# Optimization experiments

Measured on AMD Instinct MI355X. Metric: run time of the kernel, lower is better.

The kernel has to match this reference:

```python
import jax, jax.numpy as jnp
import numpy as np

B, NNODE, E = 262144, 5, 8
NF, EF, D, ED = 7, 2, 16, 4
L = 4  # num_convs
INV = 1.0 / np.sqrt(1.0 + 1e-5)  # BN eval with running_mean=0, running_var=1


def setup_inputs() -> dict:
    key = jax.random.key(0)
    ks = iter(jax.random.split(key, 64))
    r = lambda shape, s=0.1: s * jax.random.normal(next(ks), shape, dtype=jnp.float32)
    g = lambda shape: 1.0 + 0.1 * jax.random.normal(next(ks), shape, dtype=jnp.float32)
    inp = {}
    inp['node_feat'] = jax.random.normal(next(ks), (B, NNODE, NF), dtype=jnp.float32)
    inp['edge_feat'] = jax.random.normal(next(ks), (B, E, EF), dtype=jnp.float32)
    inp['edge_index'] = jax.random.randint(next(ks), (2, E), 0, NNODE)
    # embeddings
    inp['W_ne'] = r((NF, D)); inp['b_ne'] = r((D,))
    inp['g_ne'] = g((NNODE,)); inp['be_ne'] = r((NNODE,))
    inp['W_ee'] = r((EF, ED)); inp['b_ee'] = r((ED,))
    # conv layers (stacked over L)
    inp['msg_W1'] = r((L, 2 * D + ED, D)); inp['msg_b1'] = r((L, D))
    inp['msg_W2'] = r((L, D, D)); inp['msg_b2'] = r((L, D))
    inp['upd_W1'] = r((L, 2 * D, D)); inp['upd_b1'] = r((L, D))
    inp['upd_g1'] = g((L, NNODE)); inp['upd_be1'] = r((L, NNODE))
    inp['upd_W2'] = r((L, D, D)); inp['upd_b2'] = r((L, D))
    inp['upd_g2'] = g((L, NNODE)); inp['upd_be2'] = r((L, NNODE))
    # pool
    inp['Wp'] = r((NNODE * D, D)); inp['bp'] = r((D,))
    inp['gp'] = g((D,)); inp['bep'] = r((D,))
    # MLP head
    inp['mlp_W1'] = r((D, 64)); inp['mlp_b1'] = r((64,)); inp['mlp_g1'] = g((64,)); inp['mlp_be1'] = r((64,))
    inp['mlp_W2'] = r((64, 64)); inp['mlp_b2'] = r((64,)); inp['mlp_g2'] = g((64,)); inp['mlp_be2'] = r((64,))
    inp['mlp_W3'] = r((64, 64)); inp['mlp_b3'] = r((64,)); inp['mlp_g3'] = g((64,)); inp['mlp_be3'] = r((64,))
    inp['mlp_W4'] = r((64, 1)); inp['mlp_b4'] = r((1,))
    return inp


def _bn5(x, gam, bet):  # x: [B,5,D], BatchNorm1d(5) eval over channel dim 1
    return gam[None, :, None] * (x * INV) + bet[None, :, None]


def _bnc(x, gam, bet):  # x: [N,C]
    return gam * (x * INV) + bet


def reference(node_feat, edge_feat, edge_index, W_ne, b_ne, g_ne, be_ne, W_ee, b_ee,
              msg_W1, msg_b1, msg_W2, msg_b2, upd_W1, upd_b1, upd_g1, upd_be1,
              upd_W2, upd_b2, upd_g2, upd_be2, Wp, bp, gp, bep,
              mlp_W1, mlp_b1, mlp_g1, mlp_be1, mlp_W2, mlp_b2, mlp_g2, mlp_be2,
              mlp_W3, mlp_b3, mlp_g3, mlp_be3, mlp_W4, mlp_b4):
    src, dst = edge_index[0], edge_index[1]
    x = _bn5(node_feat @ W_ne + b_ne, g_ne, be_ne)          # [B,5,D]
    ea = edge_feat @ W_ee + b_ee                             # [B,E,ED]
    cnt = jnp.zeros((NNODE,), jnp.float32).at[dst].add(1.0)
    denom = jnp.clip(cnt, 1.0)[None, :, None]
    for l in range(L):
        h_i = x[:, dst, :]                                   # [B,E,D] dest gather
        h_j = x[:, src, :]                                   # [B,E,D] source gather
        m = jnp.concatenate([h_i, h_j, ea], axis=-1)         # [B,E,2D+ED]
        m = jax.nn.sigmoid(m @ msg_W1[l] + msg_b1[l])
        m = jax.nn.sigmoid(m @ msg_W2[l] + msg_b2[l])        # [B,E,D]
        agg = jnp.zeros_like(x).at[:, dst, :].add(m) / denom  # mean scatter -> [B,5,D]
        u = jnp.concatenate([x, agg], axis=-1)               # [B,5,2D]
        u = jax.nn.sigmoid(_bn5(u @ upd_W1[l] + upd_b1[l], upd_g1[l], upd_be1[l]))
        u = jax.nn.sigmoid(_bn5(u @ upd_W2[l] + upd_b2[l], upd_g2[l], upd_be2[l]))
        x = x + u                                            # residual
    p = x.reshape(x.shape[0], NNODE * D)                     # concat of 5 node slots
    p = jax.nn.sigmoid(_bnc(p @ Wp + bp, gp, bep))
    p = jax.nn.sigmoid(_bnc(p @ mlp_W1 + mlp_b1, mlp_g1, mlp_be1))
    p = jax.nn.sigmoid(_bnc(p @ mlp_W2 + mlp_b2, mlp_g2, mlp_be2))
    p = jax.nn.sigmoid(_bnc(p @ mlp_W3 + mlp_b3, mlp_g3, mlp_be3))
    return p @ mlp_W4 + mlp_b4                               # [B,1]
```

## Files before the change

### kernel.cpp

```cpp
#include <hip/hip_runtime.h>

#define NT 256
#define GPB 64
#define NB 262144
#define NCOL 66
#define ROWS 128
#define INVC 0.9999950000374997f

typedef __attribute__((ext_vector_type(8))) short bf8;
typedef __attribute__((ext_vector_type(4))) float f4;

struct P {
  const float* node_feat; const float* edge_feat; const int* ei;
  const float* W_ne; const float* b_ne; const float* g_ne; const float* be_ne;
  const float* W_ee; const float* b_ee;
  const float* msg_W1; const float* msg_b1; const float* msg_W2; const float* msg_b2;
  const float* upd_W1; const float* upd_b1; const float* upd_g1; const float* upd_be1;
  const float* upd_W2; const float* upd_b2; const float* upd_g2; const float* upd_be2;
  const float* Wp; const float* bp; const float* gp; const float* bep;
  const float* mW1; const float* mb1; const float* mg1; const float* mbe1;
  const float* mW2; const float* mb2; const float* mg2; const float* mbe2;
  const float* mW3; const float* mb3; const float* mg3; const float* mbe3;
  const float* mW4; const float* mb4;
  float* out;
};

__device__ __forceinline__ float sigm(float x) {
  return __builtin_amdgcn_rcpf(1.0f + __expf(-x));
}

__device__ __forceinline__ float bff(short s) {
  return __builtin_bit_cast(float, ((unsigned)(unsigned short)s) << 16);
}

struct F2 { bf8 h, l; };

__device__ __forceinline__ F2 pack2(const float (&v)[8]) {
  F2 r;
#pragma unroll
  for (int i = 0; i < 8; i++) {
    short hi = (short)(__builtin_bit_cast(unsigned, v[i]) >> 16);
    r.h[i] = hi;
    float res = v[i] - bff(hi);
    r.l[i] = (short)(__builtin_bit_cast(unsigned, res) >> 16);
  }
  return r;
}

__device__ __forceinline__ f4 mm(const F2& a, const F2& b, f4 c) {
  c = __builtin_amdgcn_mfma_f32_16x16x32_bf16(a.l, b.h, c, 0, 0, 0);
  c = __builtin_amdgcn_mfma_f32_16x16x32_bf16(a.h, b.l, c, 0, 0, 0);
  c = __builtin_amdgcn_mfma_f32_16x16x32_bf16(a.h, b.h, c, 0, 0, 0);
  return c;
}

template <int KV>
__device__ __forceinline__ F2 packB(const float* W, int LD, int q, int n) {
  float v[8];
#pragma unroll
  for (int i = 0; i < 8; i++) {
    const int kq = 8 * q + i;
    v[i] = (kq < KV) ? W[kq * LD + n] : 0.f;
  }
  return pack2(v);
}

__device__ __forceinline__ F2 packAr(const float* xb, int row0) {
  float v[8];
#pragma unroll
  for (int i = 0; i < 8; i++) v[i] = xb[(row0 + i) * NCOL];
  return pack2(v);
}
__device__ __forceinline__ F2 packA16(const float* xb, int rowbase, int q) {
  float v[8];
#pragma unroll
  for (int i = 0; i < 8; i++) {
    const int k = 8 * q + i;
    v[i] = (k < 16) ? xb[(rowbase + k) * NCOL] : 0.f;
  }
  return pack2(v);
}

__device__ __forceinline__ void wrD(float* dst, f4 d) {
  *(float2*)dst = float2{d[0], d[1]};
  *(float2*)(dst + 2) = float2{d[2], d[3]};
}

__device__ __forceinline__ f4 splat4(float b) { return f4{b, b, b, b}; }

__global__ __launch_bounds__(NT, 1) void gnn_kernel(P pp) {
  __shared__ float xs[ROWS][NCOL];

  const int t = threadIdx.x;
  const int w = t >> 6;
  const int l = t & 63;
  const int q = l >> 4;
  const int m16 = l & 15;
  const int col = w * 16 + m16;
  const int cD = w * 16 + 4 * q;
  const int gbase = blockIdx.x * GPB + w * 16;

  const float* xb = &xs[0][col];
  const f4 z4 = {0.f, 0.f, 0.f, 0.f};

  int se_[8], de_[8];
#pragma unroll
  for (int e = 0; e < 8; e++) {
    se_[e] = __builtin_amdgcn_readfirstlane(pp.ei[e]);
    de_[e] = __builtin_amdgcn_readfirstlane(pp.ei[8 + e]);
  }
  float dr_[5];
#pragma unroll
  for (int n = 0; n < 5; n++) {
    int c = 0;
#pragma unroll
    for (int e = 0; e < 8; e++) c += (de_[e] == n) ? 1 : 0;
    dr_[n] = 1.0f / (float)(c > 1 ? c : 1);
  }

  {
    F2 Bne = packB<7>(pp.W_ne, 16, q, m16);
#pragma unroll 1
    for (int n = 0; n < 5; n++) {
      float v[8];
#pragma unroll
      for (int i = 0; i < 8; i++) {
        const int k = 8 * q + i;
        v[i] = (k < 7) ? pp.node_feat[(size_t)(gbase + m16) * 35 + n * 7 + k] : 0.f;
      }
      F2 a = pack2(v);
      f4 d = mm(a, Bne, z4);
      const float gn = pp.g_ne[n] * INVC, bn = pp.be_ne[n];
      f4 o;
#pragma unroll
      for (int r = 0; r < 4; r++) o[r] = fmaf(gn, d[r], bn);
      wrD(&xs[n * 16 + m16][cD], o);
    }
  }

#pragma unroll 1
  for (int l4 = 0; l4 < 4; l4++) {
    const float* mW1 = pp.msg_W1 + l4 * 576;
    F2 B1a = packB<32>(mW1, 16, q, m16);
    F2 B1e = packB<4>(mW1 + 512, 16, q, m16);
    F2 B2  = packB<16>(pp.msg_W2 + l4 * 256, 16, q, m16);
    F2 BU1 = packB<32>(pp.upd_W1 + l4 * 512, 16, q, m16);
    F2 BU2 = packB<16>(pp.upd_W2 + l4 * 256, 16, q, m16);
    const float mb1n = pp.msg_b1[l4 * 16 + m16];
    const float mb2n = pp.msg_b2[l4 * 16 + m16];
    const float ub1n = pp.upd_b1[l4 * 16 + m16];
    const float ub2n = pp.upd_b2[l4 * 16 + m16];

    f4 agg[5];
#pragma unroll
    for (int n = 0; n < 5; n++) agg[n] = z4;

#pragma unroll 1
    for (int e = 0; e < 8; e++) {
      const int se = se_[e], de = de_[e];

      float v[8] = {0.f, 0.f, 0.f, 0.f, 0.f, 0.f, 0.f, 0.f};
      if (q == 0) {
        const float* ef = pp.edge_feat + (size_t)(gbase + m16) * 16 + 2 * e;
        const float e0 = ef[0], e1 = ef[1];
#pragma unroll
        for (int j = 0; j < 4; j++)
          v[j] = fmaf(e0, pp.W_ee[j], fmaf(e1, pp.W_ee[4 + j], pp.b_ee[j]));
      }
      F2 aea = pack2(v);

      f4 c1 = splat4(mb1n);
      c1 = mm(aea, B1e, c1);
      const int rowH = (q < 2) ? de * 16 + 8 * q : se * 16 + 8 * (q - 2);
      F2 ah = packAr(xb, rowH);
      c1 = mm(ah, B1a, c1);
#pragma unroll
      for (int r = 0; r < 4; r++) c1[r] = sigm(c1[r]);
      wrD(&xs[80 + m16][cD], c1);
      F2 am = packA16(xb, 80, q);

      f4 c2 = splat4(mb2n);
      c2 = mm(am, B2, c2);
#pragma unroll
      for (int r = 0; r < 4; r++) {
        const float vv = sigm(c2[r]);
        agg[0][r] += (de == 0) ? vv : 0.f;
        agg[1][r] += (de == 1) ? vv : 0.f;
        agg[2][r] += (de == 2) ? vv : 0.f;
        agg[3][r] += (de == 3) ? vv : 0.f;
        agg[4][r] += (de == 4) ? vv : 0.f;
      }
    }

#pragma unroll
    for (int nn = 0; nn < 5; nn++) {
      const float dr = dr_[nn];
      f4 av;
#pragma unroll
      for (int r = 0; r < 4; r++) av[r] = agg[nn][r] * dr;
      wrD(&xs[80 + m16][cD], av);
      const int rowU = (q < 2) ? nn * 16 + 8 * q : 80 + 8 * (q - 2);
      F2 au = packAr(xb, rowU);
      f4 c = splat4(ub1n);
      c = mm(au, BU1, c);
      const float G1 = pp.upd_g1[l4 * 5 + nn] * INVC;
      const float Bb1 = pp.upd_be1[l4 * 5 + nn];
#pragma unroll
      for (int r = 0; r < 4; r++) c[r] = sigm(fmaf(G1, c[r], Bb1));
      wrD(&xs[80 + m16][cD], c);
      F2 a2 = packA16(xb, 80, q);
      f4 c2 = splat4(ub2n);
      c2 = mm(a2, BU2, c2);
      const float G2 = pp.upd_g2[l4 * 5 + nn] * INVC;
      const float Bb2 = pp.upd_be2[l4 * 5 + nn];
      float* xp = &xs[nn * 16 + m16][cD];
      float2 x01 = *(float2*)xp;
      float2 x23 = *(float2*)(xp + 2);
      x01.x += sigm(fmaf(G2, c2[0], Bb2));
      x01.y += sigm(fmaf(G2, c2[1], Bb2));
      x23.x += sigm(fmaf(G2, c2[2], Bb2));
      x23.y += sigm(fmaf(G2, c2[3], Bb2));
      *(float2*)xp = x01;
      *(float2*)(xp + 2) = x23;
    }
  }

  {
    f4 c = splat4(pp.bp[m16]);
    F2 a0 = packAr(xb, 8 * q);
    F2 b0 = packB<32>(pp.Wp, 16, q, m16);
    c = mm(a0, b0, c);
    F2 a1 = packAr(xb, 32 + 8 * q);
    F2 b1 = packB<32>(pp.Wp + 512, 16, q, m16);
    c = mm(a1, b1, c);
    F2 a2 = packA16(xb, 64, q);
    F2 b2 = packB<16>(pp.Wp + 1024, 16, q, m16);
    c = mm(a2, b2, c);
    const float gpn = pp.gp[m16] * INVC, bepn = pp.bep[m16];
    f4 o;
#pragma unroll
    for (int r = 0; r < 4; r++) o[r] = sigm(fmaf(gpn, c[r], bepn));
    wrD(&xs[80 + m16][cD], o);
  }

  {
    F2 a = packA16(xb, 80, q);
#pragma unroll 1
    for (int nt = 0; nt < 4; nt++) {
      const int nb = nt * 16 + m16;
      F2 b = packB<16>(pp.mW1 + nt * 16, 64, q, m16);
      f4 c = splat4(pp.mb1[nb]);
      c = mm(a, b, c);
      const float g = pp.mg1[nb] * INVC, be = pp.mbe1[nb];
      f4 o;
#pragma unroll
      for (int r = 0; r < 4; r++) o[r] = sigm(fmaf(g, c[r], be));
      wrD(&xs[nt * 16 + m16][cD], o);
    }
  }
  {
    F2 a0 = packAr(xb, 8 * q);
    F2 a1 = packAr(xb, 32 + 8 * q);
#pragma unroll 1
    for (int nt = 0; nt < 4; nt++) {
      const int nb = nt * 16 + m16;
      F2 b0 = packB<32>(pp.mW2 + nt * 16, 64, q, m16);
      F2 b1 = packB<32>(pp.mW2 + 32 * 64 + nt * 16, 64, q, m16);
      f4 c = splat4(pp.mb2[nb]);
      c = mm(a0, b0, c);
      c = mm(a1, b1, c);
      const float g = pp.mg2[nb] * INVC, be = pp.mbe2[nb];
      f4 o;
#pragma unroll
      for (int r = 0; r < 4; r++) o[r] = sigm(fmaf(g, c[r], be));
      wrD(&xs[64 + nt * 16 + m16][cD], o);
    }
  }
  {
    F2 a0 = packAr(xb, 64 + 8 * q);
    F2 a1 = packAr(xb, 96 + 8 * q);
#pragma unroll 1
    for (int nt = 0; nt < 4; nt++) {
      const int nb = nt * 16 + m16;
      F2 b0 = packB<32>(pp.mW3 + nt * 16, 64, q, m16);
      F2 b1 = packB<32>(pp.mW3 + 32 * 64 + nt * 16, 64, q, m16);
      f4 c = splat4(pp.mb3[nb]);
      c = mm(a0, b0, c);
      c = mm(a1, b1, c);
      const float g = pp.mg3[nb] * INVC, be = pp.mbe3[nb];
      f4 o;
#pragma unroll
      for (int r = 0; r < 4; r++) o[r] = sigm(fmaf(g, c[r], be));
      wrD(&xs[nt * 16 + m16][cD], o);
    }
  }
  {
    float s = 0.f;
#pragma unroll
    for (int j = 0; j < 16; j++)
      s = fmaf(xs[q * 16 + j][col], pp.mW4[q * 16 + j], s);
    s += __shfl_down(s, 32);
    s += __shfl_down(s, 16);
    if (l < 16) pp.out[gbase + m16] = s + pp.mb4[0];
  }
}

extern "C" void kernel_launch(void* const* d_in, const int* in_sizes, int n_in,
                              void* d_out, int out_size, void* d_ws, size_t ws_size,
                              hipStream_t stream) {
  P p;
  p.node_feat = (const float*)d_in[0];
  p.edge_feat = (const float*)d_in[1];
  p.ei        = (const int*)d_in[2];
  p.W_ne  = (const float*)d_in[3];  p.b_ne  = (const float*)d_in[4];
  p.g_ne  = (const float*)d_in[5];  p.be_ne = (const float*)d_in[6];
  p.W_ee  = (const float*)d_in[7];  p.b_ee  = (const float*)d_in[8];
  p.msg_W1 = (const float*)d_in[9];  p.msg_b1 = (const float*)d_in[10];
  p.msg_W2 = (const float*)d_in[11]; p.msg_b2 = (const float*)d_in[12];
  p.upd_W1 = (const float*)d_in[13]; p.upd_b1 = (const float*)d_in[14];
  p.upd_g1 = (const float*)d_in[15]; p.upd_be1 = (const float*)d_in[16];
  p.upd_W2 = (const float*)d_in[17]; p.upd_b2 = (const float*)d_in[18];
  p.upd_g2 = (const float*)d_in[19]; p.upd_be2 = (const float*)d_in[20];
  p.Wp  = (const float*)d_in[21]; p.bp  = (const float*)d_in[22];
  p.gp  = (const float*)d_in[23]; p.bep = (const float*)d_in[24];
  p.mW1 = (const float*)d_in[25]; p.mb1 = (const float*)d_in[26];
  p.mg1 = (const float*)d_in[27]; p.mbe1 = (const float*)d_in[28];
  p.mW2 = (const float*)d_in[29]; p.mb2 = (const float*)d_in[30];
  p.mg2 = (const float*)d_in[31]; p.mbe2 = (const float*)d_in[32];
  p.mW3 = (const float*)d_in[33]; p.mb3 = (const float*)d_in[34];
  p.mg3 = (const float*)d_in[35]; p.mbe3 = (const float*)d_in[36];
  p.mW4 = (const float*)d_in[37]; p.mb4 = (const float*)d_in[38];
  p.out = (float*)d_out;

  hipLaunchKernelGGL(gnn_kernel, dim3(NB / GPB), dim3(NT), 0, stream, p);
}
```

Measured before the change: 337.6 us.

## Store activations in shared memory as pre-split bf16 hi/lo pairs

Shared-memory activations are now stored as packed 32-bit words holding the bf16 high part and the bf16 residual, split once at write time. Building an MFMA fragment then needs only byte permutes instead of a full float-to-bf16x2 split per element on every read. packA16 also skips the loads for the zero-padded quads. The residual state x is kept in this packed form, so each update adds precision loss (effectively about 16 mantissa bits). The row stride also changes from 66 to 64, which may alter LDS bank-conflict behaviour.

Measured after the change: 385.6 us. +14.2%, slower.

```diff
diff --git a/kernel.cpp b/kernel.cpp
--- a/kernel.cpp
+++ b/kernel.cpp
@@ -3,12 +3,14 @@
 #define NT 256
 #define GPB 64
 #define NB 262144
-#define NCOL 66
+#define NCOL 64
 #define ROWS 128
 #define INVC 0.9999950000374997f
 
 typedef __attribute__((ext_vector_type(8))) short bf8;
 typedef __attribute__((ext_vector_type(4))) float f4;
+typedef unsigned int u32;
+typedef __attribute__((ext_vector_type(4))) unsigned int u32x4;
 
 struct P {
   const float* node_feat; const float* edge_feat; const int* ei;
@@ -29,22 +31,44 @@
   return __builtin_amdgcn_rcpf(1.0f + __expf(-x));
 }
 
-__device__ __forceinline__ float bff(short s) {
-  return __builtin_bit_cast(float, ((unsigned)(unsigned short)s) << 16);
+__device__ __forceinline__ u32 pk(float v) {
+  u32 u = __builtin_bit_cast(u32, v);
+  u32 hi = u & 0xFFFF0000u;
+  float res = v - __builtin_bit_cast(float, hi);
+  return hi | (__builtin_bit_cast(u32, res) >> 16);
+}
+__device__ __forceinline__ float upk(u32 p) {
+  return __builtin_bit_cast(float, p & 0xFFFF0000u) +
+         __builtin_bit_cast(float, p << 16);
 }
 
 struct F2 { bf8 h, l; };
 
+__device__ __forceinline__ F2 fragFromU32(const u32 (&x)[8]) {
+  u32x4 H, L;
+#pragma unroll
+  for (int i = 0; i < 4; i++) {
+    H[i] = __builtin_amdgcn_perm(x[2 * i + 1], x[2 * i], 0x07060302u);
+    L[i] = __builtin_amdgcn_perm(x[2 * i + 1], x[2 * i], 0x05040100u);
+  }
+  F2 r;
+  r.h = __builtin_bit_cast(bf8, H);
+  r.l = __builtin_bit_cast(bf8, L);
+  return r;
+}
+
+__device__ __forceinline__ F2 zeroF2() {
+  F2 r;
+  r.h = __builtin_bit_cast(bf8, (u32x4)(0u));
+  r.l = r.h;
+  return r;
+}
+
 __device__ __forceinline__ F2 pack2(const float (&v)[8]) {
-  F2 r;
-#pragma unroll
-  for (int i = 0; i < 8; i++) {
-    short hi = (short)(__builtin_bit_cast(unsigned, v[i]) >> 16);
-    r.h[i] = hi;
-    float res = v[i] - bff(hi);
-    r.l[i] = (short)(__builtin_bit_cast(unsigned, res) >> 16);
-  }
-  return r;
+  u32 x[8];
+#pragma unroll
+  for (int i = 0; i < 8; i++) x[i] = pk(v[i]);
+  return fragFromU32(x);
 }
 
 __device__ __forceinline__ f4 mm(const F2& a, const F2& b, f4 c) {
@@ -65,31 +89,26 @@
   return pack2(v);
 }
 
-__device__ __forceinline__ F2 packAr(const float* xb, int row0) {
-  float v[8];
-#pragma unroll
-  for (int i = 0; i < 8; i++) v[i] = xb[(row0 + i) * NCOL];
-  return pack2(v);
-}
-__device__ __forceinline__ F2 packA16(const float* xb, int rowbase, int q) {
-  float v[8];
-#pragma unroll
-  for (int i = 0; i < 8; i++) {
-    const int k = 8 * q + i;
-    v[i] = (k < 16) ? xb[(rowbase + k) * NCOL] : 0.f;
-  }
-  return pack2(v);
-}
-
-__device__ __forceinline__ void wrD(float* dst, f4 d) {
-  *(float2*)dst = float2{d[0], d[1]};
-  *(float2*)(dst + 2) = float2{d[2], d[3]};
+__device__ __forceinline__ F2 packAr(const u32* xb, int row0) {
+  u32 x[8];
+#pragma unroll
+  for (int i = 0; i < 8; i++) x[i] = xb[(row0 + i) * NCOL];
+  return fragFromU32(x);
+}
+__device__ __forceinline__ F2 packA16(const u32* xb, int rowbase, int q) {
+  if (q < 2) return packAr(xb, rowbase + 8 * q);
+  return zeroF2();
+}
+
+__device__ __forceinline__ void wrDp(u32* dst, f4 d) {
+  *(uint2*)dst = uint2{pk(d[0]), pk(d[1])};
+  *(uint2*)(dst + 2) = uint2{pk(d[2]), pk(d[3])};
 }
 
 __device__ __forceinline__ f4 splat4(float b) { return f4{b, b, b, b}; }
 
 __global__ __launch_bounds__(NT, 1) void gnn_kernel(P pp) {
-  __shared__ float xs[ROWS][NCOL];
+  __shared__ u32 xs32[ROWS][NCOL];
 
   const int t = threadIdx.x;
   const int w = t >> 6;
@@ -100,7 +119,7 @@
   const int cD = w * 16 + 4 * q;
   const int gbase = blockIdx.x * GPB + w * 16;
 
-  const float* xb = &xs[0][col];
+  const u32* xb = &xs32[0][col];
   const f4 z4 = {0.f, 0.f, 0.f, 0.f};
 
   int se_[8], de_[8];
@@ -134,7 +153,7 @@
       f4 o;
 #pragma unroll
       for (int r = 0; r < 4; r++) o[r] = fmaf(gn, d[r], bn);
-      wrD(&xs[n * 16 + m16][cD], o);
+      wrDp(&xs32[n * 16 + m16][cD], o);
     }
   }
 
@@ -176,7 +195,7 @@
       c1 = mm(ah, B1a, c1);
 #pragma unroll
       for (int r = 0; r < 4; r++) c1[r] = sigm(c1[r]);
-      wrD(&xs[80 + m16][cD], c1);
+      wrDp(&xs32[80 + m16][cD], c1);
       F2 am = packA16(xb, 80, q);
 
       f4 c2 = splat4(mb2n);
@@ -198,7 +217,7 @@
       f4 av;
 #pragma unroll
       for (int r = 0; r < 4; r++) av[r] = agg[nn][r] * dr;
-      wrD(&xs[80 + m16][cD], av);
+      wrDp(&xs32[80 + m16][cD], av);
       const int rowU = (q < 2) ? nn * 16 + 8 * q : 80 + 8 * (q - 2);
       F2 au = packAr(xb, rowU);
       f4 c = splat4(ub1n);
@@ -207,21 +226,21 @@
       const float Bb1 = pp.upd_be1[l4 * 5 + nn];
 #pragma unroll
       for (int r = 0; r < 4; r++) c[r] = sigm(fmaf(G1, c[r], Bb1));
-      wrD(&xs[80 + m16][cD], c);
+      wrDp(&xs32[80 + m16][cD], c);
       F2 a2 = packA16(xb, 80, q);
       f4 c2 = splat4(ub2n);
       c2 = mm(a2, BU2, c2);
       const float G2 = pp.upd_g2[l4 * 5 + nn] * INVC;
       const float Bb2 = pp.upd_be2[l4 * 5 + nn];
-      float* xp = &xs[nn * 16 + m16][cD];
-      float2 x01 = *(float2*)xp;
-      float2 x23 = *(float2*)(xp + 2);
-      x01.x += sigm(fmaf(G2, c2[0], Bb2));
-      x01.y += sigm(fmaf(G2, c2[1], Bb2));
-      x23.x += sigm(fmaf(G2, c2[2], Bb2));
-      x23.y += sigm(fmaf(G2, c2[3], Bb2));
-      *(float2*)xp = x01;
-      *(float2*)(xp + 2) = x23;
+      u32* xp = &xs32[nn * 16 + m16][cD];
+      uint2 a01 = *(uint2*)xp;
+      uint2 a23 = *(uint2*)(xp + 2);
+      a01.x = pk(upk(a01.x) + sigm(fmaf(G2, c2[0], Bb2)));
+      a01.y = pk(upk(a01.y) + sigm(fmaf(G2, c2[1], Bb2)));
+      a23.x = pk(upk(a23.x) + sigm(fmaf(G2, c2[2], Bb2)));
+      a23.y = pk(upk(a23.y) + sigm(fmaf(G2, c2[3], Bb2)));
+      *(uint2*)xp = a01;
+      *(uint2*)(xp + 2) = a23;
     }
   }
 
@@ -240,7 +259,7 @@
     f4 o;
 #pragma unroll
     for (int r = 0; r < 4; r++) o[r] = sigm(fmaf(gpn, c[r], bepn));
-    wrD(&xs[80 + m16][cD], o);
+    wrDp(&xs32[80 + m16][cD], o);
   }
 
   {
@@ -255,7 +274,7 @@
       f4 o;
 #pragma unroll
       for (int r = 0; r < 4; r++) o[r] = sigm(fmaf(g, c[r], be));
-      wrD(&xs[nt * 16 + m16][cD], o);
+      wrDp(&xs32[nt * 16 + m16][cD], o);
     }
   }
   {
@@ -273,7 +292,7 @@
       f4 o;
 #pragma unroll
       for (int r = 0; r < 4; r++) o[r] = sigm(fmaf(g, c[r], be));
-      wrD(&xs[64 + nt * 16 + m16][cD], o);
+      wrDp(&xs32[64 + nt * 16 + m16][cD], o);
     }
   }
   {
@@ -291,14 +310,14 @@
       f4 o;
 #pragma unroll
       for (int r = 0; r < 4; r++) o[r] = sigm(fmaf(g, c[r], be));
-      wrD(&xs[nt * 16 + m16][cD], o);
+      wrDp(&xs32[nt * 16 + m16][cD], o);
     }
   }
   {
     float s = 0.f;
 #pragma unroll
     for (int j = 0; j < 16; j++)
-      s = fmaf(xs[q * 16 + j][col], pp.mW4[q * 16 + j], s);
+      s = fmaf(upk(xs32[q * 16 + j][col]), pp.mW4[q * 16 + j], s);
     s += __shfl_down(s, 32);
     s += __shfl_down(s, 16);
     if (l < 16) pp.out[gbase + m16] = s + pp.mb4[0];
```
